# Kernel optimization log

Hardware: AMD Instinct MI355X
Metric: run time of the kernel (lower is better)

The kernel has to match this reference:

```python
import jax, jax.numpy as jnp
import numpy as np

B, S, H, D, R = 16, 2048, 1024, 64, 2048  # batch, seq_len, hidden, inner_dim, num_relations


def setup_inputs() -> dict:
    key = jax.random.key(0)
    k1, k2, k3, k4 = jax.random.split(key, 4)
    last_hidden_state = jax.random.normal(k1, (B, S, H), dtype=jnp.float32)
    W = jax.random.normal(k2, (H, 2 * D), dtype=jnp.float32) * (H ** -0.5)
    b = jnp.zeros((2 * D,), dtype=jnp.float32)
    position_ids = jnp.tile(jnp.arange(S, dtype=jnp.int32), (B, 1))
    relations_idx = jax.random.randint(k3, (B, R, 4), 0, S, dtype=jnp.int32)
    labels_mask = (jax.random.uniform(k4, (B, R)) > 0.1).astype(jnp.float32)
    return {
        'last_hidden_state': last_hidden_state,
        'W': W,
        'b': b,
        'position_ids': position_ids,
        'relations_idx': relations_idx,
        'labels_mask': labels_mask,
    }


def reference(last_hidden_state, W, b, position_ids, relations_idx, labels_mask):
    # linear projection -> split into q/k halves
    outputs = last_hidden_state @ W + b            # [B,S,2D]
    qw, kw = outputs[..., :D], outputs[..., D:]    # each [B,S,D]

    # RoPE (interleaved sin/cos layout matching torch stack+reshape)
    inv_freq = jnp.power(10000.0, -2.0 * jnp.arange(D // 2, dtype=jnp.float32) / D)
    ang = position_ids[..., None].astype(jnp.float32) * inv_freq  # [B,S,D/2]
    sin_pos = jnp.repeat(jnp.sin(ang), 2, axis=-1)  # [B,S,D]
    cos_pos = jnp.repeat(jnp.cos(ang), 2, axis=-1)  # [B,S,D]

    def rotate(x):
        x2 = jnp.stack([-x[..., 1::2], x[..., ::2]], axis=-1).reshape(x.shape)
        return x * cos_pos + x2 * sin_pos

    qw = rotate(qw)
    kw = rotate(kw)

    # gather span endpoints: relations_idx[...,k] -> [B,R], take along seq axis
    def gather(x, idx):
        return jnp.take_along_axis(x, idx[..., None], axis=1)  # [B,R,D]

    sub_qw = jnp.concatenate([gather(qw, relations_idx[:, :, 0]),
                              gather(qw, relations_idx[:, :, 1])], axis=-1)  # [B,R,2D]
    obj_kw = jnp.concatenate([gather(kw, relations_idx[:, :, 2]),
                              gather(kw, relations_idx[:, :, 3])], axis=-1)  # [B,R,2D]

    logits = jnp.sum(sub_qw * obj_kw, axis=-1)     # [B,R]
    logits = logits + (1.0 - labels_mask) * -1e12
    return logits / jnp.sqrt(jnp.float32(D))
```

## Files before the change

### kernel.cpp

```cpp
#include <hip/hip_runtime.h>
#include <hip/hip_bf16.h>
#include <cstdint>

#define B_ 16
#define S_ 2048
#define H_ 1024
#define D_ 64
#define R_ 2048
#define M_ (B_*S_)
#define N_ 128
#define NC_ 16

typedef short short8 __attribute__((ext_vector_type(8)));
typedef float f32x4  __attribute__((ext_vector_type(4)));

__device__ __forceinline__ unsigned short f2bf(float f) {
    unsigned u = __builtin_bit_cast(unsigned, f);
    u += 0x7FFFu + ((u >> 16) & 1u);
    return (unsigned short)(u >> 16);
}
__device__ __forceinline__ unsigned pk2(float a, float b) {
    return (unsigned)f2bf(a) | ((unsigned)f2bf(b) << 16);
}
__device__ __forceinline__ float bflo(unsigned u) {
    return __builtin_bit_cast(float, u << 16);
}
__device__ __forceinline__ float bfhi(unsigned u) {
    return __builtin_bit_cast(float, u & 0xFFFF0000u);
}

typedef const __attribute__((address_space(1))) void gvoid_t;
typedef __attribute__((address_space(3))) void lvoid_t;
__device__ __forceinline__ void gload16(const void* g, void* l) {
    __builtin_amdgcn_global_load_lds((gvoid_t*)g, (lvoid_t*)l, 16, 0, 0);
}

__global__ void build_wt(const float* __restrict__ W, unsigned short* __restrict__ Wt) {
    int o = blockIdx.x * 256 + threadIdx.x;
    int n = o >> 10, k = o & 1023;
    Wt[o] = f2bf(W[k * N_ + n]);
}

__launch_bounds__(256, 2)
__global__ void gemm_rope(const float* __restrict__ A,
                          const unsigned short* __restrict__ Wt,
                          const float* __restrict__ bias,
                          const int* __restrict__ pos_ids,
                          unsigned* __restrict__ qk)
{
    __shared__ __align__(16) float          abuf[2][64 * 64];
    __shared__ __align__(16) unsigned short wbuf[2][N_ * 64];

    const int tid  = threadIdx.x;
    const int wave = tid >> 6, lane = tid & 63;
    const int ln15 = lane & 15, quad = lane >> 4, key = ln15 & 7;
    const int m0   = blockIdx.x * 64;

    const float* a_g[4];
    const unsigned short* w_g[4];
    int a_lo[4], w_lo[4];
    #pragma unroll
    for (int t = 0; t < 4; t++) {
        const int rl = wave * 16 + t * 4 + (lane >> 4);
        a_g[t]  = A + (size_t)(m0 + rl) * H_ + (((lane & 15) ^ (rl & 7)) << 2);
        a_lo[t] = (wave * 16 + t * 4) * 64;
        const int n = (wave * 4 + t) * 8 + (lane >> 3);
        w_g[t]  = Wt + (size_t)n * 1024 + (((lane & 7) ^ (n & 7)) << 3);
        w_lo[t] = (wave * 4 + t) * 8 * 64;
    }

    f32x4 acc[8];
    #pragma unroll
    for (int j = 0; j < 8; j++) acc[j] = (f32x4)0.f;

    #pragma unroll
    for (int t = 0; t < 4; t++) {
        gload16(a_g[t], &abuf[0][a_lo[t]]);
        gload16(w_g[t], &wbuf[0][w_lo[t]]);
    }

    const float* ab_lane_base;
    for (int kc = 0; kc < NC_; kc++) {
        __syncthreads();
        if (kc + 1 < NC_) {
            const int nb = (kc + 1) & 1;
            #pragma unroll
            for (int t = 0; t < 4; t++) {
                gload16(a_g[t] + (kc + 1) * 64, &abuf[nb][a_lo[t]]);
                gload16(w_g[t] + (kc + 1) * 64, &wbuf[nb][w_lo[t]]);
            }
        }
        const int cb = kc & 1;
        ab_lane_base = &abuf[cb][(wave * 16 + ln15) * 64];
        #pragma unroll
        for (int ks = 0; ks < 2; ks++) {
            const int g0 = ks * 8 + quad * 2;
            f32x4 r0 = *(const f32x4*)(ab_lane_base + ((g0 ^ key) << 2));
            f32x4 r1 = *(const f32x4*)(ab_lane_base + (((g0 + 1) ^ key) << 2));
            int4 ai;
            ai.x = (int)pk2(r0[0], r0[1]);
            ai.y = (int)pk2(r0[2], r0[3]);
            ai.z = (int)pk2(r1[0], r1[1]);
            ai.w = (int)pk2(r1[2], r1[3]);
            const short8 af = __builtin_bit_cast(short8, ai);
            const int p = ((ks * 4 + quad) ^ key) << 3;
            #pragma unroll
            for (int j = 0; j < 8; j++) {
                const short8 bf = *(const short8*)(&wbuf[cb][(j * 16 + ln15) * 64 + p]);
                acc[j] = __builtin_amdgcn_mfma_f32_16x16x32_bf16(af, bf, acc[j], 0, 0, 0);
            }
        }
    }

    const int rbase = m0 + wave * 16 + quad * 4;
    float bv[8], invr[4];
    #pragma unroll
    for (int j = 0; j < 8; j++) bv[j] = bias[j * 16 + ln15];
    #pragma unroll
    for (int jj = 0; jj < 4; jj++) {
        const float fi = (float)((jj * 16 + ln15) >> 1);
        invr[jj] = exp2f(fi * -0.41524101186092029f) * 0.15915494309189535f;
    }
    const bool odd = (ln15 & 1);
    #pragma unroll
    for (int reg = 0; reg < 4; reg++) {
        const int r = rbase + reg;
        const float pos = (float)pos_ids[r];
        #pragma unroll
        for (int j = 0; j < 8; j++) {
            const int c = j * 16 + ln15;
            float v = acc[j][reg] + bv[j];
            float p = __shfl_xor(v, 1, 64);
            float fr = __builtin_amdgcn_fractf(pos * invr[j & 3]);
            float s  = __builtin_amdgcn_sinf(fr);
            float co = __builtin_amdgcn_cosf(fr);
            float outv = odd ? fmaf(v, co, p * s) : fmaf(v, co, -p * s);
            float po = __shfl_xor(outv, 1, 64);
            if (!odd)
                qk[(size_t)r * 64 + (c >> 1)] = pk2(outv, po);
        }
    }
}

__global__ void gather_dot(const unsigned* __restrict__ qk, const int* __restrict__ rel,
                           const float* __restrict__ mask, float* __restrict__ out)
{
    const int w    = (blockIdx.x * 256 + threadIdx.x) >> 6;
    const int lane = threadIdx.x & 63;
    const int b    = w >> 11;
    const int4 id4 = ((const int4*)rel)[w];
    const unsigned* base = qk + (size_t)b * S_ * 64;
    const int rq  = (lane < 32) ? id4.x : id4.y;
    const int rk  = (lane < 32) ? id4.z : id4.w;
    const int col = lane & 31;
    const unsigned uq = base[(size_t)rq * 64 + col];
    const unsigned uk = base[(size_t)rk * 64 + 32 + col];
    float v = bflo(uq) * bflo(uk) + bfhi(uq) * bfhi(uk);
    #pragma unroll
    for (int off = 32; off; off >>= 1) v += __shfl_xor(v, off, 64);
    if (lane == 0)
        out[w] = (v + (1.0f - mask[w]) * -1e12f) * 0.125f;
}

extern "C" void kernel_launch(void* const* d_in, const int* in_sizes, int n_in,
                              void* d_out, int out_size, void* d_ws, size_t ws_size,
                              hipStream_t stream) {
    const float* lhs  = (const float*)d_in[0];
    const float* W    = (const float*)d_in[1];
    const float* bias = (const float*)d_in[2];
    const int*   pos  = (const int*)d_in[3];
    const int*   rel  = (const int*)d_in[4];
    const float* mask = (const float*)d_in[5];
    float* out = (float*)d_out;

    unsigned short* Wt = (unsigned short*)d_ws;
    unsigned* qk = (unsigned*)((char*)d_ws + (size_t)N_ * H_ * 2);

    build_wt<<<512, 256, 0, stream>>>(W, Wt);
    gemm_rope<<<512, 256, 0, stream>>>(lhs, Wt, bias, pos, qk);
    gather_dot<<<8192, 256, 0, stream>>>(qk, rel, mask, out);
}
```

Measured before the change: 220.6 us.

## Replace LDS-staged GEMM with direct-from-global single-wave 16x64 tiles

The GEMM no longer stages A and W tiles through double-buffered LDS with async global-to-LDS loads. Each 64-thread block now computes a 16-row by 64-column tile, loading fp32 activations and bf16 weights straight into registers, and the two column halves of a row block are scheduled next to each other so the shared A rows can be reused from L2. The fp32-to-bf16 conversion of A switches from round-to-nearest to truncation, which is cheaper but slightly less accurate. The risk is that A is now read twice from global memory and there is no explicit prefetch pipeline, so latency hiding depends on occupancy and the cache.

```diff
diff --git a/kernel.cpp b/kernel.cpp
--- a/kernel.cpp
+++ b/kernel.cpp
@@ -9,7 +9,6 @@
 #define R_ 2048
 #define M_ (B_*S_)
 #define N_ 128
-#define NC_ 16
 
 typedef short short8 __attribute__((ext_vector_type(8)));
 typedef float f32x4  __attribute__((ext_vector_type(4)));
@@ -22,17 +21,15 @@
 __device__ __forceinline__ unsigned pk2(float a, float b) {
     return (unsigned)f2bf(a) | ((unsigned)f2bf(b) << 16);
 }
+__device__ __forceinline__ unsigned pkt(float a, float b) {
+    return (__builtin_bit_cast(unsigned, a) >> 16) |
+           (__builtin_bit_cast(unsigned, b) & 0xFFFF0000u);
+}
 __device__ __forceinline__ float bflo(unsigned u) {
     return __builtin_bit_cast(float, u << 16);
 }
 __device__ __forceinline__ float bfhi(unsigned u) {
     return __builtin_bit_cast(float, u & 0xFFFF0000u);
-}
-
-typedef const __attribute__((address_space(1))) void gvoid_t;
-typedef __attribute__((address_space(3))) void lvoid_t;
-__device__ __forceinline__ void gload16(const void* g, void* l) {
-    __builtin_amdgcn_global_load_lds((gvoid_t*)g, (lvoid_t*)l, 16, 0, 0);
 }
 
 __global__ void build_wt(const float* __restrict__ W, unsigned short* __restrict__ Wt) {
@@ -41,85 +38,62 @@
     Wt[o] = f2bf(W[k * N_ + n]);
 }
 
-__launch_bounds__(256, 2)
+__launch_bounds__(64, 4)
 __global__ void gemm_rope(const float* __restrict__ A,
                           const unsigned short* __restrict__ Wt,
                           const float* __restrict__ bias,
                           const int* __restrict__ pos_ids,
                           unsigned* __restrict__ qk)
 {
-    __shared__ __align__(16) float          abuf[2][64 * 64];
-    __shared__ __align__(16) unsigned short wbuf[2][N_ * 64];
+    const int lane = threadIdx.x;
+    const int ln15 = lane & 15, quad = lane >> 4;
+    const int idx  = blockIdx.x;
+    const int u    = idx & 15;
+    const int rb   = (idx >> 4) * 8 + (u & 7);
+    const int ch   = u >> 3;
+    const int m0   = rb * 16;
+    const int nb   = ch * 64;
 
-    const int tid  = threadIdx.x;
-    const int wave = tid >> 6, lane = tid & 63;
-    const int ln15 = lane & 15, quad = lane >> 4, key = ln15 & 7;
-    const int m0   = blockIdx.x * 64;
+    const char* a_base = (const char*)(A + (size_t)(m0 + ln15) * H_) + quad * 32;
+    const char* w_base[4];
+    #pragma unroll
+    for (int j = 0; j < 4; j++)
+        w_base[j] = (const char*)(Wt + (size_t)(nb + j * 16 + ln15) * H_) + quad * 16;
 
-    const float* a_g[4];
-    const unsigned short* w_g[4];
-    int a_lo[4], w_lo[4];
+    f32x4 acc[4];
     #pragma unroll
-    for (int t = 0; t < 4; t++) {
-        const int rl = wave * 16 + t * 4 + (lane >> 4);
-        a_g[t]  = A + (size_t)(m0 + rl) * H_ + (((lane & 15) ^ (rl & 7)) << 2);
-        a_lo[t] = (wave * 16 + t * 4) * 64;
-        const int n = (wave * 4 + t) * 8 + (lane >> 3);
-        w_g[t]  = Wt + (size_t)n * 1024 + (((lane & 7) ^ (n & 7)) << 3);
-        w_lo[t] = (wave * 4 + t) * 8 * 64;
-    }
-
-    f32x4 acc[8];
-    #pragma unroll
-    for (int j = 0; j < 8; j++) acc[j] = (f32x4)0.f;
+    for (int j = 0; j < 4; j++) acc[j] = (f32x4)0.f;
 
     #pragma unroll
-    for (int t = 0; t < 4; t++) {
-        gload16(a_g[t], &abuf[0][a_lo[t]]);
-        gload16(w_g[t], &wbuf[0][w_lo[t]]);
-    }
-
-    const float* ab_lane_base;
-    for (int kc = 0; kc < NC_; kc++) {
-        __syncthreads();
-        if (kc + 1 < NC_) {
-            const int nb = (kc + 1) & 1;
-            #pragma unroll
-            for (int t = 0; t < 4; t++) {
-                gload16(a_g[t] + (kc + 1) * 64, &abuf[nb][a_lo[t]]);
-                gload16(w_g[t] + (kc + 1) * 64, &wbuf[nb][w_lo[t]]);
-            }
-        }
-        const int cb = kc & 1;
-        ab_lane_base = &abuf[cb][(wave * 16 + ln15) * 64];
+    for (int kc = 0; kc < 16; kc++) {
+        const int ao = kc * 256;
+        const int wo = kc * 128;
         #pragma unroll
         for (int ks = 0; ks < 2; ks++) {
-            const int g0 = ks * 8 + quad * 2;
-            f32x4 r0 = *(const f32x4*)(ab_lane_base + ((g0 ^ key) << 2));
-            f32x4 r1 = *(const f32x4*)(ab_lane_base + (((g0 + 1) ^ key) << 2));
+            f32x4 a0 = *(const f32x4*)(a_base + ao + ks * 128);
+            f32x4 a1 = *(const f32x4*)(a_base + ao + ks * 128 + 16);
             int4 ai;
-            ai.x = (int)pk2(r0[0], r0[1]);
-            ai.y = (int)pk2(r0[2], r0[3]);
-            ai.z = (int)pk2(r1[0], r1[1]);
-            ai.w = (int)pk2(r1[2], r1[3]);
+            ai.x = (int)pkt(a0[0], a0[1]);
+            ai.y = (int)pkt(a0[2], a0[3]);
+            ai.z = (int)pkt(a1[0], a1[1]);
+            ai.w = (int)pkt(a1[2], a1[3]);
             const short8 af = __builtin_bit_cast(short8, ai);
-            const int p = ((ks * 4 + quad) ^ key) << 3;
             #pragma unroll
-            for (int j = 0; j < 8; j++) {
-                const short8 bf = *(const short8*)(&wbuf[cb][(j * 16 + ln15) * 64 + p]);
+            for (int j = 0; j < 4; j++) {
+                const short8 bf = *(const short8*)(w_base[j] + wo + ks * 64);
                 acc[j] = __builtin_amdgcn_mfma_f32_16x16x32_bf16(af, bf, acc[j], 0, 0, 0);
             }
         }
     }
 
-    const int rbase = m0 + wave * 16 + quad * 4;
-    float bv[8], invr[4];
+    const int rbase = m0 + quad * 4;
+    float bv[4], invr[4];
     #pragma unroll
-    for (int j = 0; j < 8; j++) bv[j] = bias[j * 16 + ln15];
+    for (int j = 0; j < 4; j++) bv[j] = bias[nb + j * 16 + ln15];
     #pragma unroll
-    for (int jj = 0; jj < 4; jj++) {
-        const float fi = (float)((jj * 16 + ln15) >> 1);
-        invr[jj] = exp2f(fi * -0.41524101186092029f) * 0.15915494309189535f;
+    for (int j = 0; j < 4; j++) {
+        const float fi = (float)((j * 16 + ln15) >> 1);
+        invr[j] = exp2f(fi * -0.41524101186092029f) * 0.15915494309189535f;
     }
     const bool odd = (ln15 & 1);
     #pragma unroll
@@ -127,17 +101,16 @@
         const int r = rbase + reg;
         const float pos = (float)pos_ids[r];
         #pragma unroll
-        for (int j = 0; j < 8; j++) {
-            const int c = j * 16 + ln15;
+        for (int j = 0; j < 4; j++) {
             float v = acc[j][reg] + bv[j];
             float p = __shfl_xor(v, 1, 64);
-            float fr = __builtin_amdgcn_fractf(pos * invr[j & 3]);
+            float fr = __builtin_amdgcn_fractf(pos * invr[j]);
             float s  = __builtin_amdgcn_sinf(fr);
             float co = __builtin_amdgcn_cosf(fr);
             float outv = odd ? fmaf(v, co, p * s) : fmaf(v, co, -p * s);
             float po = __shfl_xor(outv, 1, 64);
             if (!odd)
-                qk[(size_t)r * 64 + (c >> 1)] = pk2(outv, po);
+                qk[(size_t)r * 64 + ch * 32 + j * 8 + (ln15 >> 1)] = pk2(outv, po);
         }
     }
 }
@@ -177,6 +150,6 @@
     unsigned* qk = (unsigned*)((char*)d_ws + (size_t)N_ * H_ * 2);
 
     build_wt<<<512, 256, 0, stream>>>(W, Wt);
-    gemm_rope<<<512, 256, 0, stream>>>(lhs, Wt, bias, pos, qk);
+    gemm_rope<<<4096, 64, 0, stream>>>(lhs, Wt, bias, pos, qk);
     gather_dot<<<8192, 256, 0, stream>>>(qk, rel, mask, out);
 }
```

New measurement: 269.2 us. 1.22x slower.
